# Performance work log

Hardware: AMD Instinct MI355X
Metric: run time of the kernel (lower is better)

The kernel has to match this reference:

```python
import jax, jax.numpy as jnp
import numpy as np

N_HEADS = 16
THETA = 10000.0


def _rope_cos_sin(seq_len, head_dim):
    # freqs_cis = exp(i * pos * theta^(-2j/d)), shape (seq_len, head_dim//2)
    inv_freq = 1.0 / (THETA ** (np.arange(0, head_dim, 2, dtype=np.float32) / head_dim))
    ang = np.arange(seq_len, dtype=np.float32)[:, None] * inv_freq[None, :]
    return jnp.asarray(np.cos(ang)), jnp.asarray(np.sin(ang))


def _apply_rope(t, cos, sin):
    # t: [B, S, H, hd]; rotate consecutive pairs as complex numbers
    B, S, H, hd = t.shape
    pairs = t.reshape(B, S, H, hd // 2, 2)
    r, i = pairs[..., 0], pairs[..., 1]
    c = cos[None, :, None, :]  # [1, S, 1, hd//2]
    s = sin[None, :, None, :]
    out_r = r * c - i * s
    out_i = r * s + i * c
    return jnp.stack([out_r, out_i], axis=-1).reshape(B, S, H, hd)


def setup_inputs() -> dict:
    key = jax.random.key(0)
    ks = jax.random.split(key, 5)
    B, S, D = 2, 2048, 2048
    scale = 1.0 / np.sqrt(D)
    return {
        "x": jax.random.normal(ks[0], (B, S, D), dtype=jnp.float32),
        "wq": jax.random.normal(ks[1], (D, D), dtype=jnp.float32) * scale,
        "wk": jax.random.normal(ks[2], (D, D), dtype=jnp.float32) * scale,
        "wv": jax.random.normal(ks[3], (D, D), dtype=jnp.float32) * scale,
        "wo": jax.random.normal(ks[4], (D, D), dtype=jnp.float32) * scale,
    }


def reference(x, wq, wk, wv, wo):
    B, S, D = x.shape
    H = N_HEADS
    hd = D // H
    cos, sin = _rope_cos_sin(S, hd)

    xq = (x @ wq.T).reshape(B, S, H, hd)
    xk = (x @ wk.T).reshape(B, S, H, hd)
    xv = (x @ wv.T).reshape(B, S, H, hd)

    xq = _apply_rope(xq, cos, sin)
    xk = _apply_rope(xk, cos, sin)

    # [B, H, S, S] scores, full (non-causal) softmax as in the source
    scores = jnp.einsum("bqhd,bkhd->bhqk", xq, xk) / jnp.sqrt(jnp.float32(hd))
    attn = jax.nn.softmax(scores, axis=-1)
    out = jnp.einsum("bhqk,bkhd->bqhd", attn, xv).reshape(B, S, D)
    return out @ wo.T
```

## Files before the change

### kernel.cpp

```cpp
#include <hip/hip_runtime.h>
#include <hip/hip_bf16.h>
#include <stdint.h>


typedef __attribute__((ext_vector_type(4))) float f32x4;
typedef __attribute__((ext_vector_type(8))) short bf16x8;

typedef __attribute__((address_space(3))) unsigned int lds_u32;
typedef __attribute__((address_space(1))) const unsigned int gbl_u32;

__device__ __forceinline__ void async16(const void* g, void* l) {
  __builtin_amdgcn_global_load_lds((gbl_u32*)g, (lds_u32*)l, 16, 0, 0);
}

__device__ __forceinline__ float bf_to_f(unsigned short u) {
  union { unsigned int i; float f; } v; v.i = ((unsigned int)u) << 16; return v.f;
}
__device__ __forceinline__ unsigned short f_to_bf(float f) {
  union { float f; unsigned int i; } v; v.f = f;
  unsigned int r = v.i + 0x7FFFu + ((v.i >> 16) & 1u);
  return (unsigned short)(r >> 16);
}
__device__ __forceinline__ unsigned int cvt_pk_bf16(float lo, float hi) {
  unsigned int r;
  asm("v_cvt_pk_bf16_f32 %0, %1, %2" : "=v"(r) : "v"(lo), "v"(hi));
  return r;
}

#define B_ 2
#define S_ 2048
#define D_ 2048
#define H_ 16
#define HD_ 128

__global__ __launch_bounds__(256) void conv_all(const float* __restrict__ x,
                                                const float* __restrict__ wq,
                                                const float* __restrict__ wk,
                                                const float* __restrict__ wv,
                                                const float* __restrict__ wo,
                                                unsigned short* __restrict__ xb,
                                                unsigned short* __restrict__ wb) {
  int i = blockIdx.x * 256 + threadIdx.x;
  const float* s;
  unsigned short* d;
  int off;
  if (i < 2097152) {
    s = x; d = xb; off = i;
  } else {
    int j = i - 2097152;
    int t = j >> 20;
    off = j & 1048575;
    s = (t == 0) ? wq : (t == 1) ? wk : (t == 2) ? wv : wo;
    d = wb + (size_t)t * 4194304;
  }
  float4 v = ((const float4*)s)[off];
  uint2 o;
  o.x = (unsigned int)f_to_bf(v.x) | ((unsigned int)f_to_bf(v.y) << 16);
  o.y = (unsigned int)f_to_bf(v.z) | ((unsigned int)f_to_bf(v.w) << 16);
  ((uint2*)d)[off] = o;
}

__global__ __launch_bounds__(256) void rope_table_kernel(float* __restrict__ cosT,
                                                         float* __restrict__ sinT) {
  int i = blockIdx.x * 256 + threadIdx.x;
  int s = i >> 6, j = i & 63;
  float inv = powf(10000.0f, -(float)(2 * j) * (1.0f / 128.0f));
  float ang = (float)s * inv;
  float sv, cv;
  sincosf(ang, &sv, &cv);
  cosT[i] = cv;
  sinT[i] = sv;
}

__global__ __launch_bounds__(256, 3) void qkv_gemm(const unsigned short* __restrict__ A,
                                                   const unsigned short* __restrict__ W,
                                                   unsigned short* __restrict__ Qb,
                                                   unsigned short* __restrict__ Kb,
                                                   unsigned short* __restrict__ Vtb,
                                                   const float* __restrict__ cosT,
                                                   const float* __restrict__ sinT) {
  __shared__ unsigned short sA[128 * 32];
  __shared__ unsigned short sB[128 * 32];
  const int K = 2048, N = 2048;
  const int tid = threadIdx.x;
  const int l = tid & 63, wv = tid >> 6;
  const int lane15 = l & 15, lhi = l >> 4;
  const int wm = wv >> 1, wn = wv & 1;
  const int bm = blockIdx.x, bn = blockIdx.y;
  const int sector = bn >> 4, bnl = bn & 15;
  const unsigned short* Ag = A + (size_t)bm * 128 * K;
  const unsigned short* Bg = W + (size_t)bn * 128 * K;

  f32x4 acc[4][4];
  const f32x4 zero = {0.f, 0.f, 0.f, 0.f};
#pragma unroll
  for (int i = 0; i < 4; i++)
#pragma unroll
    for (int j = 0; j < 4; j++) acc[i][j] = zero;

  for (int k0 = 0; k0 < K; k0 += 32) {
    __syncthreads();
#pragma unroll
    for (int i = 0; i < 2; i++) {
      int c = i * 256 + tid;
      int row = c >> 2, col = (c & 3) << 3;
      async16(Ag + (size_t)row * K + k0 + col, &sA[c * 8]);
      async16(Bg + (size_t)row * K + k0 + col, &sB[c * 8]);
    }
    __syncthreads();

    bf16x8 af[4], bfr[4];
#pragma unroll
    for (int i = 0; i < 4; i++)
      af[i] = *(const bf16x8*)&sA[(wm * 64 + i * 16 + lane15) * 32 + lhi * 8];
#pragma unroll
    for (int j = 0; j < 4; j++)
      bfr[j] = *(const bf16x8*)&sB[(wn * 64 + j * 16 + lane15) * 32 + lhi * 8];
#pragma unroll
    for (int i = 0; i < 4; i++)
#pragma unroll
      for (int j = 0; j < 4; j++)
        acc[i][j] = __builtin_amdgcn_mfma_f32_16x16x32_bf16(af[i], bfr[j], acc[i][j], 0, 0, 0);
  }

#pragma unroll
  for (int i = 0; i < 4; i++) {
    int m0 = bm * 128 + wm * 64 + i * 16 + lhi * 4;
#pragma unroll
    for (int j = 0; j < 4; j++) {
      int n = bnl * 128 + wn * 64 + j * 16 + lane15;
      if (sector == 0) {
#pragma unroll
        for (int r = 0; r < 4; r++) Qb[(size_t)(m0 + r) * N + n] = f_to_bf(acc[i][j][r]);
      } else if (sector == 1) {
        int s0 = m0 & (S_ - 1);
        int jp = (n & (HD_ - 1)) >> 1;
        int odd = n & 1;
#pragma unroll
        for (int r = 0; r < 4; r++) {
          float own = acc[i][j][r];
          float prt = __shfl_xor(own, 1);
          float c = cosT[(s0 + r) * 64 + jp];
          float sn = sinT[(s0 + r) * 64 + jp];
          float outv = odd ? fmaf(prt, sn, own * c) : own * c - prt * sn;
          Kb[(size_t)(m0 + r) * N + n] = f_to_bf(outv);
        }
      } else {
        int s0 = m0 & (S_ - 1);
        size_t row = (size_t)((m0 >> 11) * D_ + n);
        uint2 st;
        st.x = (unsigned int)f_to_bf(acc[i][j][0]) | ((unsigned int)f_to_bf(acc[i][j][1]) << 16);
        st.y = (unsigned int)f_to_bf(acc[i][j][2]) | ((unsigned int)f_to_bf(acc[i][j][3]) << 16);
        *(uint2*)(Vtb + row * S_ + s0) = st;
      }
    }
  }
}

__global__ __launch_bounds__(256, 3) void gemm_out(const unsigned short* __restrict__ A,
                                                   const unsigned short* __restrict__ Bm,
                                                   float* __restrict__ Cf) {
  __shared__ unsigned short sA[128 * 32];
  __shared__ unsigned short sB[128 * 32];
  const int K = 2048, N = 2048;
  const int tid = threadIdx.x;
  const int l = tid & 63, wv = tid >> 6;
  const int lane15 = l & 15, lhi = l >> 4;
  const int wm = wv >> 1, wn = wv & 1;
  const int bm = blockIdx.x, bn = blockIdx.y;
  const unsigned short* Ag = A + (size_t)bm * 128 * K;
  const unsigned short* Bg = Bm + (size_t)bn * 128 * K;

  f32x4 acc[4][4];
  const f32x4 zero = {0.f, 0.f, 0.f, 0.f};
#pragma unroll
  for (int i = 0; i < 4; i++)
#pragma unroll
    for (int j = 0; j < 4; j++) acc[i][j] = zero;

  for (int k0 = 0; k0 < K; k0 += 32) {
    __syncthreads();
#pragma unroll
    for (int i = 0; i < 2; i++) {
      int c = i * 256 + tid;
      int row = c >> 2, col = (c & 3) << 3;
      async16(Ag + (size_t)row * K + k0 + col, &sA[c * 8]);
      async16(Bg + (size_t)row * K + k0 + col, &sB[c * 8]);
    }
    __syncthreads();

    bf16x8 af[4], bfr[4];
#pragma unroll
    for (int i = 0; i < 4; i++)
      af[i] = *(const bf16x8*)&sA[(wm * 64 + i * 16 + lane15) * 32 + lhi * 8];
#pragma unroll
    for (int j = 0; j < 4; j++)
      bfr[j] = *(const bf16x8*)&sB[(wn * 64 + j * 16 + lane15) * 32 + lhi * 8];
#pragma unroll
    for (int i = 0; i < 4; i++)
#pragma unroll
      for (int j = 0; j < 4; j++)
        acc[i][j] = __builtin_amdgcn_mfma_f32_16x16x32_bf16(af[i], bfr[j], acc[i][j], 0, 0, 0);
  }

#pragma unroll
  for (int i = 0; i < 4; i++) {
    int m0 = bm * 128 + wm * 64 + i * 16 + lhi * 4;
#pragma unroll
    for (int j = 0; j < 4; j++) {
      int n = bn * 128 + wn * 64 + j * 16 + lane15;
#pragma unroll
      for (int r = 0; r < 4; r++) Cf[(size_t)(m0 + r) * N + n] = acc[i][j][r];
    }
  }
}

__global__ __launch_bounds__(512, 2) void attn_kernel(const unsigned short* __restrict__ Q,
                                                      const unsigned short* __restrict__ K,
                                                      const unsigned short* __restrict__ Vt,
                                                      unsigned short* __restrict__ ctx,
                                                      const float* __restrict__ cosT,
                                                      const float* __restrict__ sinT) {
  __shared__ unsigned short sK[2][64 * 128];
  __shared__ unsigned short sV[2][128 * 64];
  const int tid = threadIdx.x, l = tid & 63, w = tid >> 6;
  const int lane15 = l & 15, lhi = l >> 4;
  const int bh = blockIdx.x * 4 + (blockIdx.y >> 3);
  const int qt = blockIdx.y & 7;
  const int b = bh >> 4, h = bh & 15;
  const int q0 = qt * 256;
  const unsigned short* Kg = K + ((size_t)(b * S_)) * D_ + h * HD_;
  const unsigned short* Vg = Vt + ((size_t)bh * HD_) * S_;
  const float qscale = 0.08838834764831845f * 1.44269504f;
  const float THR = 11.5415603f;

  const unsigned short* gp0;
  const unsigned short* gp1;
  const unsigned short* gp2;
  const unsigned short* gp3;
  unsigned int ldsOff[4];
  int gstride;
  if (w < 4) {
    const unsigned short* t0;
#pragma unroll
    for (int i = 0; i < 4; i++) {
      int row = w * 16 + i * 4 + (l >> 4);
      int colD = (l & 15) << 4;
      int colS = colD ^ ((row & 7) << 4);
      t0 = Kg + (size_t)row * D_ + (colS >> 1);
      if (i == 0) gp0 = t0; else if (i == 1) gp1 = t0; else if (i == 2) gp2 = t0; else gp3 = t0;
      ldsOff[i] = row * 256 + colD;
    }
    gstride = 64 * D_;
  } else {
    const unsigned short* t0;
#pragma unroll
    for (int i = 0; i < 4; i++) {
      int row = (w - 4) * 32 + i * 8 + (l >> 3);
      int colD = (l & 7) << 4;
      int colS = colD ^ ((row & 7) << 4);
      t0 = Vg + (size_t)row * S_ + (colS >> 1);
      if (i == 0) gp0 = t0; else if (i == 1) gp1 = t0; else if (i == 2) gp2 = t0; else gp3 = t0;
      ldsOff[i] = row * 128 + colD;
    }
    gstride = 64;
  }

  bf16x8 qf[2][4];
#pragma unroll
  for (int s = 0; s < 2; s++) {
    int s_q = q0 + w * 32 + s * 16 + lane15;
    const unsigned short* Qrow = Q + ((size_t)(b * S_ + s_q)) * D_ + h * HD_;
#pragma unroll
    for (int kc = 0; kc < 4; kc++) {
      int d0 = kc * 32 + lhi * 8;
      uint4 raw = *(const uint4*)(Qrow + d0);
      float4 cv = *(const float4*)(cosT + (size_t)s_q * 64 + (d0 >> 1));
      float4 sv = *(const float4*)(sinT + (size_t)s_q * 64 + (d0 >> 1));
      unsigned int u[4] = {raw.x, raw.y, raw.z, raw.w};
      float cc[4] = {cv.x, cv.y, cv.z, cv.w};
      float ss[4] = {sv.x, sv.y, sv.z, sv.w};
      unsigned int o[4];
#pragma unroll
      for (int p = 0; p < 4; p++) {
        float re = bf_to_f((unsigned short)(u[p] & 0xffffu));
        float im = bf_to_f((unsigned short)(u[p] >> 16));
        float orr = (re * cc[p] - im * ss[p]) * qscale;
        float oi = (re * ss[p] + im * cc[p]) * qscale;
        o[p] = (unsigned int)f_to_bf(orr) | ((unsigned int)f_to_bf(oi) << 16);
      }
      union { uint4 u4; bf16x8 v; } cvt;
      cvt.u4.x = o[0]; cvt.u4.y = o[1]; cvt.u4.z = o[2]; cvt.u4.w = o[3];
      qf[s][kc] = cvt.v;
    }
  }

  float mrun[2] = {-1e30f, -1e30f}, lrun[2] = {0.f, 0.f};
  const f32x4 zero = {0.f, 0.f, 0.f, 0.f};
  f32x4 oacc[2][8];
#pragma unroll
  for (int s = 0; s < 2; s++)
#pragma unroll
    for (int nf = 0; nf < 8; nf++) oacc[s][nf] = zero;

  {
    char* base = (w < 4) ? (char*)&sK[0][0] : (char*)&sV[0][0];
    async16(gp0, base + ldsOff[0]);
    async16(gp1, base + ldsOff[1]);
    async16(gp2, base + ldsOff[2]);
    async16(gp3, base + ldsOff[3]);
    gp0 += gstride; gp1 += gstride; gp2 += gstride; gp3 += gstride;
  }

  for (int t = 0; t < 32; ++t) {
    const int cur = t & 1;
    __syncthreads();
    if (t < 31) {
      char* base = (w < 4) ? (char*)&sK[cur ^ 1][0] : (char*)&sV[cur ^ 1][0];
      async16(gp0, base + ldsOff[0]);
      async16(gp1, base + ldsOff[1]);
      async16(gp2, base + ldsOff[2]);
      async16(gp3, base + ldsOff[3]);
      gp0 += gstride; gp1 += gstride; gp2 += gstride; gp3 += gstride;
    }
    const unsigned short* sKc = sK[cur];
    const unsigned short* sVc = sV[cur];

    f32x4 sacc[2][4];
#pragma unroll
    for (int s = 0; s < 2; s++)
#pragma unroll
      for (int n = 0; n < 4; n++) sacc[s][n] = zero;
    __builtin_amdgcn_s_setprio(1);
#pragma unroll
    for (int n = 0; n < 4; n++) {
      int row = n * 16 + lane15;
#pragma unroll
      for (int kc = 0; kc < 4; kc++) {
        bf16x8 kf = *(const bf16x8*)((const char*)sKc + row * 256 +
                                     ((kc * 64 + lhi * 16) ^ ((row & 7) << 4)));
        sacc[0][n] = __builtin_amdgcn_mfma_f32_16x16x32_bf16(kf, qf[0][kc], sacc[0][n], 0, 0, 0);
        sacc[1][n] = __builtin_amdgcn_mfma_f32_16x16x32_bf16(kf, qf[1][kc], sacc[1][n], 0, 0, 0);
      }
    }
    __builtin_amdgcn_s_setprio(0);

    float pmax[2];
#pragma unroll
    for (int s = 0; s < 2; s++) {
      float a0 = fmaxf(fmaxf(sacc[s][0][0], sacc[s][0][1]), fmaxf(sacc[s][0][2], sacc[s][0][3]));
      float a1 = fmaxf(fmaxf(sacc[s][1][0], sacc[s][1][1]), fmaxf(sacc[s][1][2], sacc[s][1][3]));
      float a2 = fmaxf(fmaxf(sacc[s][2][0], sacc[s][2][1]), fmaxf(sacc[s][2][2], sacc[s][2][3]));
      float a3 = fmaxf(fmaxf(sacc[s][3][0], sacc[s][3][1]), fmaxf(sacc[s][3][2], sacc[s][3][3]));
      float pm = fmaxf(fmaxf(a0, a1), fmaxf(a2, a3));
      pm = fmaxf(pm, __shfl_xor(pm, 16));
      pm = fmaxf(pm, __shfl_xor(pm, 32));
      pmax[s] = pm;
    }
    if (!__all(fmaxf(pmax[0] - mrun[0], pmax[1] - mrun[1]) <= THR)) {
#pragma unroll
      for (int s = 0; s < 2; s++) {
        float mnew = fmaxf(mrun[s], pmax[s]);
        float alpha = exp2f(mrun[s] - mnew);
        lrun[s] *= alpha;
        float af[4];
#pragma unroll
        for (int r = 0; r < 4; r++) af[r] = __shfl(alpha, lhi * 4 + r);
#pragma unroll
        for (int nf = 0; nf < 8; nf++)
#pragma unroll
          for (int r = 0; r < 4; r++) oacc[s][nf][r] *= af[r];
        mrun[s] = mnew;
      }
    }
    bf16x8 paS[2][2];
#pragma unroll
    for (int s = 0; s < 2; s++) {
      float rs = 0.f;
      float p[4][4];
#pragma unroll
      for (int n = 0; n < 4; n++)
#pragma unroll
        for (int r = 0; r < 4; r++) {
          float pv = exp2f(sacc[s][n][r] - mrun[s]);
          p[n][r] = pv;
          rs += pv;
        }
      rs += __shfl_xor(rs, 16);
      rs += __shfl_xor(rs, 32);
      lrun[s] += rs;
      unsigned int wlo[4], whi[4];
#pragma unroll
      for (int n = 0; n < 4; n++) {
        wlo[n] = cvt_pk_bf16(p[n][0], p[n][1]);
        whi[n] = cvt_pk_bf16(p[n][2], p[n][3]);
      }
#pragma unroll
      for (int kc = 0; kc < 2; kc++) {
        unsigned int A = wlo[2 * kc], Bw = whi[2 * kc];
        unsigned int C = wlo[2 * kc + 1], Dw = whi[2 * kc + 1];
        asm("v_permlane32_swap_b32 %0, %1" : "+v"(A), "+v"(C));
        asm("v_permlane16_swap_b32 %0, %1" : "+v"(A), "+v"(C));
        asm("v_permlane32_swap_b32 %0, %1" : "+v"(Bw), "+v"(Dw));
        asm("v_permlane16_swap_b32 %0, %1" : "+v"(Bw), "+v"(Dw));
        union { uint4 u4; bf16x8 v; } pk;
        pk.u4.x = A; pk.u4.y = Bw; pk.u4.z = C; pk.u4.w = Dw;
        paS[s][kc] = pk.v;
      }
    }

    __builtin_amdgcn_s_setprio(1);
#pragma unroll
    for (int nf = 0; nf < 8; nf++) {
      int row = nf * 16 + lane15;
#pragma unroll
      for (int kc = 0; kc < 2; kc++) {
        bf16x8 vf = *(const bf16x8*)((const char*)sVc + row * 128 +
                                     ((kc * 64 + lhi * 16) ^ ((row & 7) << 4)));
        oacc[0][nf] = __builtin_amdgcn_mfma_f32_16x16x32_bf16(paS[0][kc], vf, oacc[0][nf], 0, 0, 0);
        oacc[1][nf] = __builtin_amdgcn_mfma_f32_16x16x32_bf16(paS[1][kc], vf, oacc[1][nf], 0, 0, 0);
      }
    }
    __builtin_amdgcn_s_setprio(0);
  }

#pragma unroll
  for (int s = 0; s < 2; s++) {
    float inv = 1.0f / lrun[s];
    float invr[4];
#pragma unroll
    for (int r = 0; r < 4; r++) invr[r] = __shfl(inv, lhi * 4 + r);
    unsigned short* Og = ctx + ((size_t)(b * S_ + q0 + w * 32 + s * 16)) * D_ + h * HD_;
#pragma unroll
    for (int r = 0; r < 4; r++) {
      int qrow = lhi * 4 + r;
#pragma unroll
      for (int nf = 0; nf < 8; nf++)
        Og[(size_t)qrow * D_ + nf * 16 + lane15] = f_to_bf(oacc[s][nf][r] * invr[r]);
    }
  }
}

extern "C" void kernel_launch(void* const* d_in, const int* in_sizes, int n_in,
                              void* d_out, int out_size, void* d_ws, size_t ws_size,
                              hipStream_t stream) {
  (void)in_sizes; (void)n_in; (void)out_size; (void)ws_size;
  const float* x = (const float*)d_in[0];
  const float* wq = (const float*)d_in[1];
  const float* wk = (const float*)d_in[2];
  const float* wv = (const float*)d_in[3];
  const float* wo = (const float*)d_in[4];
  float* out = (float*)d_out;

  char* ws = (char*)d_ws;
  const size_t MB = 1024 * 1024;
  unsigned short* xb  = (unsigned short*)(ws + 0 * MB);
  unsigned short* wqb = (unsigned short*)(ws + 16 * MB);
  unsigned short* wob = (unsigned short*)(ws + 40 * MB);
  unsigned short* Qb  = (unsigned short*)(ws + 48 * MB);
  unsigned short* Kb  = (unsigned short*)(ws + 64 * MB);
  unsigned short* Vtb = (unsigned short*)(ws + 80 * MB);
  float* cosT = (float*)(ws + 96 * MB);
  float* sinT = (float*)(ws + 96 * MB + 524288);
  unsigned short* ctxb = xb;

  const int M = B_ * S_;

  conv_all<<<24576, 256, 0, stream>>>(x, wq, wk, wv, wo, xb, wqb);
  rope_table_kernel<<<512, 256, 0, stream>>>(cosT, sinT);

  qkv_gemm<<<dim3(M / 128, 48), 256, 0, stream>>>(xb, wqb, Qb, Kb, Vtb, cosT, sinT);

  attn_kernel<<<dim3(8, 32), 512, 0, stream>>>(Qb, Kb, Vtb, ctxb, cosT, sinT);

  gemm_out<<<dim3(M / 128, D_ / 128), 256, 0, stream>>>(ctxb, wob, out);
}
```

Baseline: 292.6 us.

## Double attention KV tile to 128 keys and raise GEMM occupancy hint

The attention kernel now processes 128 keys per iteration instead of 64, halving loop trips and barriers. K/V async load addressing, the score tile, softmax reductions and PV MFMA loops are reworked to match. It also raises the minimum-blocks hint on both GEMMs from 3 to 4. Cost: LDS doubles to 128KB per attention block, likely cutting occupancy to one block per CU. Register pressure also rises from the larger score tile, and the tighter GEMM bound may cause spills.

Measured after the change: 289.7 us. About the same (-1.0%).

```diff
diff --git a/kernel.cpp b/kernel.cpp
--- a/kernel.cpp
+++ b/kernel.cpp
@@ -32,6 +32,7 @@
 #define D_ 2048
 #define H_ 16
 #define HD_ 128
+#define KVB 128
 
 __global__ __launch_bounds__(256) void conv_all(const float* __restrict__ x,
                                                 const float* __restrict__ wq,
@@ -72,7 +73,7 @@
   sinT[i] = sv;
 }
 
-__global__ __launch_bounds__(256, 3) void qkv_gemm(const unsigned short* __restrict__ A,
+__global__ __launch_bounds__(256, 4) void qkv_gemm(const unsigned short* __restrict__ A,
                                                    const unsigned short* __restrict__ W,
                                                    unsigned short* __restrict__ Qb,
                                                    unsigned short* __restrict__ Kb,
@@ -157,7 +158,7 @@
   }
 }
 
-__global__ __launch_bounds__(256, 3) void gemm_out(const unsigned short* __restrict__ A,
+__global__ __launch_bounds__(256, 4) void gemm_out(const unsigned short* __restrict__ A,
                                                    const unsigned short* __restrict__ Bm,
                                                    float* __restrict__ Cf) {
   __shared__ unsigned short sA[128 * 32];
@@ -221,8 +222,8 @@
                                                       unsigned short* __restrict__ ctx,
                                                       const float* __restrict__ cosT,
                                                       const float* __restrict__ sinT) {
-  __shared__ unsigned short sK[2][64 * 128];
-  __shared__ unsigned short sV[2][128 * 64];
+  __shared__ unsigned short sK[2][KVB * 128];
+  __shared__ unsigned short sV[2][128 * KVB];
   const int tid = threadIdx.x, l = tid & 63, w = tid >> 6;
   const int lane15 = l & 15, lhi = l >> 4;
   const int bh = blockIdx.x * 4 + (blockIdx.y >> 3);
@@ -234,36 +235,29 @@
   const float qscale = 0.08838834764831845f * 1.44269504f;
   const float THR = 11.5415603f;
 
-  const unsigned short* gp0;
-  const unsigned short* gp1;
-  const unsigned short* gp2;
-  const unsigned short* gp3;
-  unsigned int ldsOff[4];
-  int gstride;
+  const unsigned short* gp[8];
+  unsigned int lofs[8];
+  size_t gstep;
   if (w < 4) {
-    const unsigned short* t0;
-#pragma unroll
-    for (int i = 0; i < 4; i++) {
-      int row = w * 16 + i * 4 + (l >> 4);
+#pragma unroll
+    for (int i = 0; i < 8; i++) {
+      int row = w * 32 + i * 4 + (l >> 4);
       int colD = (l & 15) << 4;
       int colS = colD ^ ((row & 7) << 4);
-      t0 = Kg + (size_t)row * D_ + (colS >> 1);
-      if (i == 0) gp0 = t0; else if (i == 1) gp1 = t0; else if (i == 2) gp2 = t0; else gp3 = t0;
-      ldsOff[i] = row * 256 + colD;
-    }
-    gstride = 64 * D_;
+      gp[i] = Kg + (size_t)row * D_ + (colS >> 1);
+      lofs[i] = row * 256 + colD;
+    }
+    gstep = (size_t)KVB * D_;
   } else {
-    const unsigned short* t0;
-#pragma unroll
-    for (int i = 0; i < 4; i++) {
-      int row = (w - 4) * 32 + i * 8 + (l >> 3);
-      int colD = (l & 7) << 4;
+#pragma unroll
+    for (int i = 0; i < 8; i++) {
+      int row = (w - 4) * 32 + i * 4 + (l >> 4);
+      int colD = (l & 15) << 4;
       int colS = colD ^ ((row & 7) << 4);
-      t0 = Vg + (size_t)row * S_ + (colS >> 1);
-      if (i == 0) gp0 = t0; else if (i == 1) gp1 = t0; else if (i == 2) gp2 = t0; else gp3 = t0;
-      ldsOff[i] = row * 128 + colD;
-    }
-    gstride = 64;
+      gp[i] = Vg + (size_t)row * S_ + (colS >> 1);
+      lofs[i] = row * 256 + colD;
+    }
+    gstep = KVB;
   }
 
   bf16x8 qf[2][4];
@@ -305,35 +299,29 @@
 
   {
     char* base = (w < 4) ? (char*)&sK[0][0] : (char*)&sV[0][0];
-    async16(gp0, base + ldsOff[0]);
-    async16(gp1, base + ldsOff[1]);
-    async16(gp2, base + ldsOff[2]);
-    async16(gp3, base + ldsOff[3]);
-    gp0 += gstride; gp1 += gstride; gp2 += gstride; gp3 += gstride;
-  }
-
-  for (int t = 0; t < 32; ++t) {
+#pragma unroll
+    for (int i = 0; i < 8; i++) { async16(gp[i], base + lofs[i]); gp[i] += gstep; }
+  }
+
+  for (int t = 0; t < S_ / KVB; ++t) {
     const int cur = t & 1;
     __syncthreads();
-    if (t < 31) {
+    if (t < S_ / KVB - 1) {
       char* base = (w < 4) ? (char*)&sK[cur ^ 1][0] : (char*)&sV[cur ^ 1][0];
-      async16(gp0, base + ldsOff[0]);
-      async16(gp1, base + ldsOff[1]);
-      async16(gp2, base + ldsOff[2]);
-      async16(gp3, base + ldsOff[3]);
-      gp0 += gstride; gp1 += gstride; gp2 += gstride; gp3 += gstride;
+#pragma unroll
+      for (int i = 0; i < 8; i++) { async16(gp[i], base + lofs[i]); gp[i] += gstep; }
     }
     const unsigned short* sKc = sK[cur];
     const unsigned short* sVc = sV[cur];
 
-    f32x4 sacc[2][4];
+    f32x4 sacc[2][8];
 #pragma unroll
     for (int s = 0; s < 2; s++)
 #pragma unroll
-      for (int n = 0; n < 4; n++) sacc[s][n] = zero;
+      for (int n = 0; n < 8; n++) sacc[s][n] = zero;
     __builtin_amdgcn_s_setprio(1);
 #pragma unroll
-    for (int n = 0; n < 4; n++) {
+    for (int n = 0; n < 8; n++) {
       int row = n * 16 + lane15;
 #pragma unroll
       for (int kc = 0; kc < 4; kc++) {
@@ -348,11 +336,12 @@
     float pmax[2];
 #pragma unroll
     for (int s = 0; s < 2; s++) {
-      float a0 = fmaxf(fmaxf(sacc[s][0][0], sacc[s][0][1]), fmaxf(sacc[s][0][2], sacc[s][0][3]));
-      float a1 = fmaxf(fmaxf(sacc[s][1][0], sacc[s][1][1]), fmaxf(sacc[s][1][2], sacc[s][1][3]));
-      float a2 = fmaxf(fmaxf(sacc[s][2][0], sacc[s][2][1]), fmaxf(sacc[s][2][2], sacc[s][2][3]));
-      float a3 = fmaxf(fmaxf(sacc[s][3][0], sacc[s][3][1]), fmaxf(sacc[s][3][2], sacc[s][3][3]));
-      float pm = fmaxf(fmaxf(a0, a1), fmaxf(a2, a3));
+      float mn[8];
+#pragma unroll
+      for (int n = 0; n < 8; n++)
+        mn[n] = fmaxf(fmaxf(sacc[s][n][0], sacc[s][n][1]), fmaxf(sacc[s][n][2], sacc[s][n][3]));
+      float pm = fmaxf(fmaxf(fmaxf(mn[0], mn[1]), fmaxf(mn[2], mn[3])),
+                       fmaxf(fmaxf(mn[4], mn[5]), fmaxf(mn[6], mn[7])));
       pm = fmaxf(pm, __shfl_xor(pm, 16));
       pm = fmaxf(pm, __shfl_xor(pm, 32));
       pmax[s] = pm;
@@ -373,30 +362,26 @@
         mrun[s] = mnew;
       }
     }
-    bf16x8 paS[2][2];
+    bf16x8 paS[2][4];
 #pragma unroll
     for (int s = 0; s < 2; s++) {
       float rs = 0.f;
-      float p[4][4];
-#pragma unroll
-      for (int n = 0; n < 4; n++)
-#pragma unroll
-        for (int r = 0; r < 4; r++) {
-          float pv = exp2f(sacc[s][n][r] - mrun[s]);
-          p[n][r] = pv;
-          rs += pv;
-        }
+      unsigned int wlo[8], whi[8];
+#pragma unroll
+      for (int n = 0; n < 8; n++) {
+        float p0 = exp2f(sacc[s][n][0] - mrun[s]);
+        float p1 = exp2f(sacc[s][n][1] - mrun[s]);
+        float p2 = exp2f(sacc[s][n][2] - mrun[s]);
+        float p3 = exp2f(sacc[s][n][3] - mrun[s]);
+        rs += (p0 + p1) + (p2 + p3);
+        wlo[n] = cvt_pk_bf16(p0, p1);
+        whi[n] = cvt_pk_bf16(p2, p3);
+      }
       rs += __shfl_xor(rs, 16);
       rs += __shfl_xor(rs, 32);
       lrun[s] += rs;
-      unsigned int wlo[4], whi[4];
-#pragma unroll
-      for (int n = 0; n < 4; n++) {
-        wlo[n] = cvt_pk_bf16(p[n][0], p[n][1]);
-        whi[n] = cvt_pk_bf16(p[n][2], p[n][3]);
-      }
-#pragma unroll
-      for (int kc = 0; kc < 2; kc++) {
+#pragma unroll
+      for (int kc = 0; kc < 4; kc++) {
         unsigned int A = wlo[2 * kc], Bw = whi[2 * kc];
         unsigned int C = wlo[2 * kc + 1], Dw = whi[2 * kc + 1];
         asm("v_permlane32_swap_b32 %0, %1" : "+v"(A), "+v"(C));
@@ -414,8 +399,8 @@
     for (int nf = 0; nf < 8; nf++) {
       int row = nf * 16 + lane15;
 #pragma unroll
-      for (int kc = 0; kc < 2; kc++) {
-        bf16x8 vf = *(const bf16x8*)((const char*)sVc + row * 128 +
+      for (int kc = 0; kc < 4; kc++) {
+        bf16x8 vf = *(const bf16x8*)((const char*)sVc + row * 256 +
                                      ((kc * 64 + lhi * 16) ^ ((row & 7) << 4)));
         oacc[0][nf] = __builtin_amdgcn_mfma_f32_16x16x32_bf16(paS[0][kc], vf, oacc[0][nf], 0, 0, 0);
         oacc[1][nf] = __builtin_amdgcn_mfma_f32_16x16x32_bf16(paS[1][kc], vf, oacc[1][nf], 0, 0, 0);
```
